# Optimization experiments

Measured on AMD Instinct MI355X. Metric: run time of the kernel, lower is better.

Reference implementation:

```python
import jax, jax.numpy as jnp
import numpy as np

N_POS = 8192          # number of positive samples
N_NEG = 4000          # negatives per positive
N_TOT = N_POS + N_POS * N_NEG


def setup_inputs() -> dict:
    key = jax.random.key(0)
    k1, k2 = jax.random.split(key)
    predict_val = jax.random.normal(k1, (N_TOT,), dtype=jnp.float32)
    # 'index' is a permutation; the module reorders predict_val by argsort(index)
    index = jax.random.permutation(k2, jnp.arange(N_TOT, dtype=jnp.int64))
    return {"predict_val": predict_val, "index": index, "num": N_NEG, "num_pos": N_POS}


def reference(predict_val, index, num, num_pos):
    # index_tuple = sorted(enumerate(index)) by value -> reorder by argsort(index)
    pv = predict_val[jnp.argsort(index)]
    pos = pv[:num_pos]                                  # [num_pos]
    neg = pv[num_pos:num_pos + num_pos * num]
    neg = neg.reshape(num_pos, num)                     # [num_pos, num]
    # rank of pos among {neg, pos} sorted descending == 1 + #(neg > pos)
    # (ties are randomly broken in the original; measure-zero for continuous scores)
    rank = 1 + jnp.sum(neg > pos[:, None], axis=-1)     # [num_pos], int
    sample_mrr = 1.0 / rank.astype(pv.dtype)            # [num_pos]
    mrr = jnp.mean(sample_mrr)
    return mrr, sample_mrr
```

## Files before the change

### kernel.cpp

```cpp
#include <hip/hip_runtime.h>


constexpr int N_POS = 8192;
constexpr int N_NEG = 4000;
constexpr int NSLOT = N_POS / 4;
constexpr int CNT_BLOCKS = 512;

typedef int   vint4   __attribute__((ext_vector_type(4)));
typedef float vfloat4 __attribute__((ext_vector_type(4)));
typedef unsigned int u32;
typedef unsigned long long u64;

__global__ __launch_bounds__(256) void scatter_pos_kernel(
    const vint4* __restrict__ idx4, const float* __restrict__ pv,
    float* __restrict__ pos, u64* __restrict__ cnt, int nvec) {
  const int gtid = blockIdx.x * 256 + threadIdx.x;
  if (gtid <= NSLOT) cnt[gtid] = 0ull;
  const int stride = gridDim.x * 256;
  int j = gtid;
#define SC_ELEM(V, JJ)                                   \
  if ((V).x < N_POS) pos[(V).x] = pv[4 * (JJ) + 0];      \
  if ((V).y < N_POS) pos[(V).y] = pv[4 * (JJ) + 1];      \
  if ((V).z < N_POS) pos[(V).z] = pv[4 * (JJ) + 2];      \
  if ((V).w < N_POS) pos[(V).w] = pv[4 * (JJ) + 3];
  for (; j + stride < nvec; j += 2 * stride) {
    vint4 a = idx4[j];
    vint4 b = idx4[j + stride];
    SC_ELEM(a, j)
    SC_ELEM(b, j + stride)
  }
  for (; j < nvec; j += stride) {
    vint4 a = idx4[j];
    SC_ELEM(a, j)
  }
#undef SC_ELEM
}

__global__ __launch_bounds__(1024) void count_kernel(
    const vint4* __restrict__ idx4, const vfloat4* __restrict__ pv4,
    const float* __restrict__ pos, u64* __restrict__ cnt,
    float* __restrict__ out, int nvec) {
  __shared__ float pos_lds[N_POS];
  __shared__ u32   lcnt[N_POS];
  __shared__ float wsum[16];
  __shared__ int is_last;
  for (int i = threadIdx.x; i < N_POS; i += 1024) {
    pos_lds[i] = pos[i];
    lcnt[i] = 0u;
  }
  __syncthreads();

  const int stride = gridDim.x * 1024;
  int j = blockIdx.x * 1024 + threadIdx.x;
#define CT_ELEM(IV, XV)                                              \
  if ((IV) >= N_POS) {                                               \
    unsigned r = (unsigned)((IV) - N_POS) / (unsigned)N_NEG;         \
    if ((XV) > pos_lds[r]) atomicAdd(&lcnt[r], 1u);                  \
  }
#define CT_VEC(V, X)                                                 \
  CT_ELEM((V).x, (X).x) CT_ELEM((V).y, (X).y)                        \
  CT_ELEM((V).z, (X).z) CT_ELEM((V).w, (X).w)
  for (; j + stride < nvec; j += 2 * stride) {
    vint4 va = idx4[j];
    vint4 vb = idx4[j + stride];
    vfloat4 xa = __builtin_nontemporal_load(&pv4[j]);
    vfloat4 xb = __builtin_nontemporal_load(&pv4[j + stride]);
    CT_VEC(va, xa)
    CT_VEC(vb, xb)
  }
  for (; j < nvec; j += stride) {
    vint4 va = idx4[j];
    vfloat4 xa = __builtin_nontemporal_load(&pv4[j]);
    CT_VEC(va, xa)
  }
#undef CT_VEC
#undef CT_ELEM
  __syncthreads();

  for (int s = threadIdx.x; s < NSLOT; s += 1024) {
    u32 c0 = lcnt[4 * s + 0], c1 = lcnt[4 * s + 1];
    u32 c2 = lcnt[4 * s + 2], c3 = lcnt[4 * s + 3];
    u64 p = (u64)c0 | ((u64)c1 << 16) | ((u64)c2 << 32) | ((u64)c3 << 48);
    if (p) atomicAdd(&cnt[s], p);
  }

  __builtin_amdgcn_s_waitcnt(0);
  __syncthreads();
  if (threadIdx.x == 0) {
    u64 prev = __hip_atomic_fetch_add(&cnt[NSLOT], 1ull, __ATOMIC_RELAXED,
                                      __HIP_MEMORY_SCOPE_AGENT);
    is_last = (prev == (u64)(gridDim.x - 1));
  }
  __syncthreads();
  if (!is_last) return;

  float lsum = 0.f;
  for (int s = threadIdx.x; s < NSLOT; s += 1024) {
    u64 p = __hip_atomic_load(&cnt[s], __ATOMIC_RELAXED,
                              __HIP_MEMORY_SCOPE_AGENT);
    float m0 = 1.0f / (float)(1u + (u32)(p & 0xFFFFu));
    float m1 = 1.0f / (float)(1u + (u32)((p >> 16) & 0xFFFFu));
    float m2 = 1.0f / (float)(1u + (u32)((p >> 32) & 0xFFFFu));
    float m3 = 1.0f / (float)(1u + (u32)((p >> 48) & 0xFFFFu));
    vfloat4 m = {m0, m1, m2, m3};
    *(vfloat4*)&out[1 + 4 * s] = m;
    lsum += m0 + m1 + m2 + m3;
  }
#pragma unroll
  for (int off = 32; off > 0; off >>= 1) lsum += __shfl_down(lsum, off, 64);
  if ((threadIdx.x & 63) == 0) wsum[threadIdx.x >> 6] = lsum;
  __syncthreads();
  if (threadIdx.x == 0) {
    float tot = 0.f;
#pragma unroll
    for (int w = 0; w < 16; ++w) tot += wsum[w];
    out[0] = tot / (float)N_POS;
  }
}

extern "C" void kernel_launch(void* const* d_in, const int* in_sizes, int n_in,
                              void* d_out, int out_size, void* d_ws, size_t ws_size,
                              hipStream_t stream) {
  const float* pv = (const float*)d_in[0];
  const int* idx = (const int*)d_in[1];
  float* out = (float*)d_out;
  float* pos = (float*)d_ws;
  u64* cnt = (u64*)((char*)d_ws + 32 * 1024);
  int nvec = in_sizes[0] / 4;

  scatter_pos_kernel<<<2048, 256, 0, stream>>>((const vint4*)idx, pv, pos,
                                               cnt, nvec);
  count_kernel<<<CNT_BLOCKS, 1024, 0, stream>>>((const vint4*)idx,
                                                (const vfloat4*)pv, pos, cnt,
                                                out, nvec);
}
```

Baseline: 286.1 us.

## Fuse scatter and count into cooperative kernel with grid barrier and register-cached row codes

Merges the two kernels into one cooperative launch. Each thread reads the index array once, scatters positive scores, and keeps the decoded row numbers packed in registers. After a software grid barrier, the count phase reuses those row codes, so the index array is not read a second time. The cost is heavy register use, a spin barrier, and fewer blocks (256) than before, with the old two-kernel path kept as a fallback if the cooperative launch fails.

```diff
diff --git a/kernel.cpp b/kernel.cpp
--- a/kernel.cpp
+++ b/kernel.cpp
@@ -4,12 +4,159 @@
 constexpr int N_POS = 8192;
 constexpr int N_NEG = 4000;
 constexpr int NSLOT = N_POS / 4;
+constexpr int GRID  = 256;
+constexpr int BLK   = 1024;
+constexpr int NTHR  = GRID * BLK;
+constexpr int NITER = 32;
 constexpr int CNT_BLOCKS = 512;
 
 typedef int   vint4   __attribute__((ext_vector_type(4)));
 typedef float vfloat4 __attribute__((ext_vector_type(4)));
 typedef unsigned int u32;
 typedef unsigned long long u64;
+
+__global__ __launch_bounds__(BLK, 4) void fused_mrr_kernel(
+    const vint4* __restrict__ idx4, const float* __restrict__ pvs,
+    float* __restrict__ pos, u64* __restrict__ cnt, u32* __restrict__ bar,
+    float* __restrict__ out, int nvec) {
+  __shared__ float pos_lds[N_POS];
+  __shared__ u32   lcnt[N_POS];
+  __shared__ float wsum[BLK / 64];
+  __shared__ int   is_last;
+  const int tid = threadIdx.x;
+  const int gid = blockIdx.x * BLK + tid;
+  const vfloat4* __restrict__ pv4 = (const vfloat4*)pvs;
+
+#pragma unroll
+  for (int i = 0; i < N_POS / BLK; ++i) lcnt[tid + i * BLK] = 0u;
+  if (gid <= NSLOT) (void)atomicExch(&cnt[gid], 0ull);
+
+  u32 code[2 * NITER];
+#define PA_ELEM(VX, PIDX, CO)                                            \
+  {                                                                      \
+    u32 c_ = ((VX) >= N_POS) ? ((u32)((VX)-N_POS) / (u32)N_NEG)          \
+                             : 0xFFFFu;                                  \
+    if ((VX) < N_POS) (void)atomicExch(&pos[VX], pvs[PIDX]);             \
+    (CO) = c_;                                                           \
+  }
+#pragma unroll
+  for (int i = 0; i < NITER; ++i) {
+    const int j = gid + i * NTHR;
+    if (j < nvec) {
+      vint4 v = __builtin_nontemporal_load(&idx4[j]);
+      u32 c0, c1, c2, c3;
+      PA_ELEM(v.x, 4 * j + 0, c0)
+      PA_ELEM(v.y, 4 * j + 1, c1)
+      PA_ELEM(v.z, 4 * j + 2, c2)
+      PA_ELEM(v.w, 4 * j + 3, c3)
+      code[2 * i]     = c0 | (c1 << 16);
+      code[2 * i + 1] = c2 | (c3 << 16);
+    } else {
+      code[2 * i]     = 0xFFFFFFFFu;
+      code[2 * i + 1] = 0xFFFFFFFFu;
+    }
+  }
+  for (int j = gid + NITER * NTHR; j < nvec; j += NTHR) {
+    vint4 v = idx4[j];
+    u32 dummy;
+    PA_ELEM(v.x, 4 * j + 0, dummy)
+    PA_ELEM(v.y, 4 * j + 1, dummy)
+    PA_ELEM(v.z, 4 * j + 2, dummy)
+    PA_ELEM(v.w, 4 * j + 3, dummy)
+    (void)dummy;
+  }
+#undef PA_ELEM
+
+  __builtin_amdgcn_s_waitcnt(0);
+  __syncthreads();
+  if (tid == 0) {
+    __hip_atomic_fetch_add(bar, 1u, __ATOMIC_RELAXED,
+                           __HIP_MEMORY_SCOPE_AGENT);
+    while (__hip_atomic_load(bar, __ATOMIC_RELAXED,
+                             __HIP_MEMORY_SCOPE_AGENT) < (u32)GRID)
+      __builtin_amdgcn_s_sleep(4);
+  }
+  __syncthreads();
+
+#pragma unroll
+  for (int i = 0; i < N_POS / BLK; ++i) {
+    const int s = tid + i * BLK;
+    pos_lds[s] = __hip_atomic_load(&pos[s], __ATOMIC_RELAXED,
+                                   __HIP_MEMORY_SCOPE_AGENT);
+  }
+  __syncthreads();
+
+#define PB_ELEM(R, XV)                                                   \
+  if ((R) < (u32)N_POS && (XV) > pos_lds[R]) atomicAdd(&lcnt[R], 1u);
+#pragma unroll
+  for (int i = 0; i < NITER; ++i) {
+    const int j = gid + i * NTHR;
+    if (j < nvec) {
+      vfloat4 x = __builtin_nontemporal_load(&pv4[j]);
+      u32 w0 = code[2 * i], w1 = code[2 * i + 1];
+      u32 r0 = w0 & 0xFFFFu, r1 = w0 >> 16;
+      u32 r2 = w1 & 0xFFFFu, r3 = w1 >> 16;
+      PB_ELEM(r0, x.x)
+      PB_ELEM(r1, x.y)
+      PB_ELEM(r2, x.z)
+      PB_ELEM(r3, x.w)
+    }
+  }
+  for (int j = gid + NITER * NTHR; j < nvec; j += NTHR) {
+    vint4 v = idx4[j];
+    vfloat4 x = pv4[j];
+    u32 r0 = (v.x >= N_POS) ? ((u32)(v.x - N_POS) / (u32)N_NEG) : 0xFFFFu;
+    u32 r1 = (v.y >= N_POS) ? ((u32)(v.y - N_POS) / (u32)N_NEG) : 0xFFFFu;
+    u32 r2 = (v.z >= N_POS) ? ((u32)(v.z - N_POS) / (u32)N_NEG) : 0xFFFFu;
+    u32 r3 = (v.w >= N_POS) ? ((u32)(v.w - N_POS) / (u32)N_NEG) : 0xFFFFu;
+    PB_ELEM(r0, x.x)
+    PB_ELEM(r1, x.y)
+    PB_ELEM(r2, x.z)
+    PB_ELEM(r3, x.w)
+  }
+#undef PB_ELEM
+  __syncthreads();
+
+  for (int s = tid; s < NSLOT; s += BLK) {
+    u32 c0 = lcnt[4 * s + 0], c1 = lcnt[4 * s + 1];
+    u32 c2 = lcnt[4 * s + 2], c3 = lcnt[4 * s + 3];
+    u64 p = (u64)c0 | ((u64)c1 << 16) | ((u64)c2 << 32) | ((u64)c3 << 48);
+    if (p) atomicAdd(&cnt[s], p);
+  }
+
+  __builtin_amdgcn_s_waitcnt(0);
+  __syncthreads();
+  if (tid == 0) {
+    u64 prev = __hip_atomic_fetch_add(&cnt[NSLOT], 1ull, __ATOMIC_RELAXED,
+                                      __HIP_MEMORY_SCOPE_AGENT);
+    is_last = (prev == (u64)(GRID - 1));
+  }
+  __syncthreads();
+  if (!is_last) return;
+
+  float lsum = 0.f;
+  for (int s = tid; s < NSLOT; s += BLK) {
+    u64 p = __hip_atomic_load(&cnt[s], __ATOMIC_RELAXED,
+                              __HIP_MEMORY_SCOPE_AGENT);
+    float m0 = 1.0f / (float)(1u + (u32)(p & 0xFFFFu));
+    float m1 = 1.0f / (float)(1u + (u32)((p >> 16) & 0xFFFFu));
+    float m2 = 1.0f / (float)(1u + (u32)((p >> 32) & 0xFFFFu));
+    float m3 = 1.0f / (float)(1u + (u32)((p >> 48) & 0xFFFFu));
+    vfloat4 m = {m0, m1, m2, m3};
+    *(vfloat4*)&out[1 + 4 * s] = m;
+    lsum += m0 + m1 + m2 + m3;
+  }
+#pragma unroll
+  for (int off = 32; off > 0; off >>= 1) lsum += __shfl_down(lsum, off, 64);
+  if ((tid & 63) == 0) wsum[tid >> 6] = lsum;
+  __syncthreads();
+  if (tid == 0) {
+    float tot = 0.f;
+#pragma unroll
+    for (int w = 0; w < BLK / 64; ++w) tot += wsum[w];
+    out[0] = tot / (float)N_POS;
+  }
+}
 
 __global__ __launch_bounds__(256) void scatter_pos_kernel(
     const vint4* __restrict__ idx4, const float* __restrict__ pv,
@@ -119,18 +266,26 @@
 }
 
 extern "C" void kernel_launch(void* const* d_in, const int* in_sizes, int n_in,
-                              void* d_out, int out_size, void* d_ws, size_t ws_size,
-                              hipStream_t stream) {
+                              void* d_out, int out_size, void* d_ws,
+                              size_t ws_size, hipStream_t stream) {
   const float* pv = (const float*)d_in[0];
-  const int* idx = (const int*)d_in[1];
+  const vint4* idx4 = (const vint4*)d_in[1];
   float* out = (float*)d_out;
   float* pos = (float*)d_ws;
   u64* cnt = (u64*)((char*)d_ws + 32 * 1024);
+  u32* bar = (u32*)((char*)d_ws + 56 * 1024);
   int nvec = in_sizes[0] / 4;
 
-  scatter_pos_kernel<<<2048, 256, 0, stream>>>((const vint4*)idx, pv, pos,
-                                               cnt, nvec);
-  count_kernel<<<CNT_BLOCKS, 1024, 0, stream>>>((const vint4*)idx,
-                                                (const vfloat4*)pv, pos, cnt,
-                                                out, nvec);
-}
+  hipMemsetAsync(bar, 0, sizeof(u32), stream);
+
+  void* args[] = {(void*)&idx4, (void*)&pv, (void*)&pos, (void*)&cnt,
+                  (void*)&bar,  (void*)&out, (void*)&nvec};
+  hipError_t e = hipLaunchCooperativeKernel((const void*)fused_mrr_kernel,
+                                            dim3(GRID), dim3(BLK), args, 0,
+                                            stream);
+  if (e != hipSuccess) {
+    scatter_pos_kernel<<<2048, 256, 0, stream>>>(idx4, pv, pos, cnt, nvec);
+    count_kernel<<<CNT_BLOCKS, 1024, 0, stream>>>(idx4, (const vfloat4*)pv,
+                                                  pos, cnt, out, nvec);
+  }
+}
```

Result: slower. 312.9 us (+9.4%).
